# Kernel tuning notes

Hardware: AMD Instinct MI355X
Metric: run time of the kernel (lower is better)

Reference implementation:

```python
import jax, jax.numpy as jnp
import numpy as np

TEMPERATURE = 0.5
B, D = 4096, 256


def setup_inputs() -> dict:
    key = jax.random.key(0)
    k1, k2 = jax.random.split(key)
    z_i = jax.random.normal(k1, (B, D), dtype=jnp.float32)
    z_j = jax.random.normal(k2, (B, D), dtype=jnp.float32)
    return {"z_i": z_i, "z_j": z_j}


def reference(z_i, z_j):
    batch = z_i.shape[0]
    n = 2 * batch
    z = jnp.concatenate([z_i, z_j], axis=0)                      # [2B, D]
    z = z / jnp.linalg.norm(z, axis=1, keepdims=True)            # L2-normalize rows
    # cosine_similarity of unit vectors == dot product -> single GEMM
    sim = jnp.einsum('id,jd->ij', z, z) / TEMPERATURE            # [2B, 2B]
    mask = jnp.eye(n, dtype=bool)
    sim = jnp.where(mask, -jnp.inf, sim)                         # mask self-similarity
    positives = jnp.concatenate(
        [jnp.diagonal(sim, offset=batch), jnp.diagonal(sim, offset=-batch)], axis=0
    )                                                            # [2B]
    loss = -positives + jax.nn.logsumexp(sim, axis=1)            # [2B]
    return loss.mean()
```

## Files before the change

kernel.cpp:

```cpp
#include <hip/hip_runtime.h>
#include <hip/hip_bf16.h>
#include <stdint.h>
#include <stddef.h>


#define B_ROWS 4096
#define D_DIM  256
#define N_ROWS 8192
#define BM 128
#define BN 128

typedef __bf16 bf16;
typedef bf16  bf16x8  __attribute__((ext_vector_type(8)));
typedef bf16  bf16x4  __attribute__((ext_vector_type(4)));
typedef float floatx4 __attribute__((ext_vector_type(4)));

__global__ __launch_bounds__(256) void normalize_kernel(
    const float* __restrict__ z_i, const float* __restrict__ z_j,
    bf16* __restrict__ zn, float* __restrict__ sumexp) {
  const int wave = threadIdx.x >> 6;
  const int lane = threadIdx.x & 63;
  const int row  = blockIdx.x * 4 + wave;
  const float* src = (row < B_ROWS) ? (z_i + (size_t)row * D_DIM)
                                    : (z_j + (size_t)(row - B_ROWS) * D_DIM);
  float4 v = ((const float4*)src)[lane];
  float ss = v.x * v.x + v.y * v.y + v.z * v.z + v.w * v.w;
  #pragma unroll
  for (int m = 1; m < 64; m <<= 1) ss += __shfl_xor(ss, m);
  const float rn = rsqrtf(ss) * 1.6986436f;
  bf16x4 o;
  o[0] = (bf16)(v.x * rn);
  o[1] = (bf16)(v.y * rn);
  o[2] = (bf16)(v.z * rn);
  o[3] = (bf16)(v.w * rn);
  ((bf16x4*)(zn + (size_t)row * D_DIM))[lane] = o;
  if (lane == 0) sumexp[row] = 0.f;
}

__global__ __launch_bounds__(512, 2) void simexp_kernel(
    const bf16* __restrict__ zn, float* __restrict__ sumexp,
    float* __restrict__ pos) {
  __shared__ __align__(16) bf16 Bs[2][BN * D_DIM];

  const int tid   = threadIdx.x;
  const int wave  = tid >> 6;
  const int lane  = tid & 63;
  const int lcol  = lane & 15;
  const int lquad = lane >> 4;
  const int wr = (wave >> 2) * 64;
  const int wc = (wave & 3) * 32;
  const int ri = blockIdx.x >> 2;
  const int cj = blockIdx.x & 3;
  const int row_base = ri * BM;
  const bool has_tail = (ri < 32 && cj >= 2);

  auto ct_of = [&](int t) { return (ri + 8 * cj + t) & 63; };

  auto stageB = [&](int buf, const bf16* src, int it0, int it1) {
    for (int it = it0; it < it1; ++it) {
      const int s   = it * 512 + tid;
      const int n   = s >> 5;
      const int kcs = s & 31;
      const int kc  = (kcs & 24) | ((kcs & 7) ^ (n & 7));
      __builtin_amdgcn_global_load_lds(
          (const __attribute__((address_space(1))) unsigned int*)
              (src + (size_t)n * D_DIM + kc * 8),
          (__attribute__((address_space(3))) unsigned int*)&Bs[buf][s * 8],
          16, 0, 0);
    }
  };

  stageB(0, zn + (size_t)row_base * D_DIM, 0, 8);
  stageB(1, zn + (size_t)ct_of(0) * BM * D_DIM, 0, 8);
  __syncthreads();

  floatx4 af[4][8];
  #pragma unroll
  for (int ti = 0; ti < 4; ++ti) {
    const int n = wr + ti * 16 + lcol;
    #pragma unroll
    for (int kq = 0; kq < 8; ++kq) {
      const int kc  = kq * 4 + lquad;
      const int kcs = (kc & 24) | ((kc & 7) ^ (n & 7));
      af[ti][kq] = *(const floatx4*)(&Bs[0][(n * 32 + kcs) * 8]);
    }
  }
  __syncthreads();

  float rowsum[4][4];
  #pragma unroll
  for (int ti = 0; ti < 4; ++ti)
    #pragma unroll
    for (int r = 0; r < 4; ++r) rowsum[ti][r] = 0.f;

#define MFMA_(A, B_, C) __builtin_amdgcn_mfma_f32_16x16x32_bf16( \
    __builtin_bit_cast(bf16x8, A), B_, C, 0, 0, 0)
#define PHASE(KQA, KQB, IT0, IT1, DO_VM)                                  \
  {                                                                       \
    bf16x8 bfrA[2], bfrB[2];                                              \
    const int kcA = (KQA) * 4 + lquad, kcB = (KQB) * 4 + lquad;           \
    _Pragma("unroll")                                                     \
    for (int tj = 0; tj < 2; ++tj) {                                      \
      const int n  = wc + tj * 16 + lcol;                                 \
      const int sA = (kcA & 24) | ((kcA & 7) ^ (n & 7));                  \
      const int sB = (kcB & 24) | ((kcB & 7) ^ (n & 7));                  \
      bfrA[tj] = *(const bf16x8*)(bbase + n * D_DIM + sA * 8);            \
      bfrB[tj] = *(const bf16x8*)(bbase + n * D_DIM + sB * 8);            \
    }                                                                     \
    stageB(sb, nsrc, IT0, IT1);                                           \
    __builtin_amdgcn_sched_barrier(0);                                    \
    __builtin_amdgcn_s_barrier();                                         \
    asm volatile("s_waitcnt lgkmcnt(0)" ::: "memory");                    \
    __builtin_amdgcn_sched_barrier(0);                                    \
    __builtin_amdgcn_s_setprio(1);                                        \
    _Pragma("unroll")                                                     \
    for (int ti = 0; ti < 4; ++ti) {                                      \
      acc[ti][0] = MFMA_(af[ti][KQA], bfrA[0], acc[ti][0]);               \
      acc[ti][1] = MFMA_(af[ti][KQA], bfrA[1], acc[ti][1]);               \
    }                                                                     \
    _Pragma("unroll")                                                     \
    for (int ti = 0; ti < 4; ++ti) {                                      \
      acc[ti][0] = MFMA_(af[ti][KQB], bfrB[0], acc[ti][0]);               \
      acc[ti][1] = MFMA_(af[ti][KQB], bfrB[1], acc[ti][1]);               \
    }                                                                     \
    __builtin_amdgcn_s_setprio(0);                                        \
    if (DO_VM) asm volatile("s_waitcnt vmcnt(0)" ::: "memory");           \
    __builtin_amdgcn_sched_barrier(0);                                    \
    __builtin_amdgcn_s_barrier();                                         \
  }

  #pragma unroll 1
  for (int t = 0; t < 8; ++t) {
    const int cb = (t ^ 1) & 1;
    const int sb = cb ^ 1;
    const bf16* bbase = &Bs[cb][0];
    const bf16* nsrc = nullptr;
    int nl = 0;
    if (t < 7) {
      nsrc = zn + (size_t)ct_of(t + 1) * BM * D_DIM;
      nl = 8;
    } else if (has_tail) {
      nsrc = zn + (size_t)((ri + 32) * BM + (cj - 2) * 64) * D_DIM;
      nl = 4;
    }
    const int nh = nl >> 1;

    floatx4 acc[4][2];
    #pragma unroll
    for (int ti = 0; ti < 4; ++ti)
      #pragma unroll
      for (int tj = 0; tj < 2; ++tj) acc[ti][tj] = floatx4{0.f, 0.f, 0.f, 0.f};

    PHASE(0, 1, 0, nh, false)
    PHASE(2, 3, nh, nl, false)
    PHASE(4, 5, 0, 0, false)
    PHASE(6, 7, 0, 0, true)

    const bool diag = (cj == 0 && t == 0);
    const int col_base = ct_of(t) * BM;
    float colsum[2] = {0.f, 0.f};
    #pragma unroll
    for (int ti = 0; ti < 4; ++ti) {
      #pragma unroll
      for (int tj = 0; tj < 2; ++tj) {
        #pragma unroll
        for (int r = 0; r < 4; ++r) {
          const float v = acc[ti][tj][r];
          float e = __builtin_amdgcn_exp2f(v);
          if (diag) {
            const int rg = row_base + wr + ti * 16 + lquad * 4 + r;
            const int cg = col_base + wc + tj * 16 + lcol;
            if (cg == rg) e = 0.f;
          }
          rowsum[ti][r] += e;
          colsum[tj]    += e;
        }
      }
    }
    if (!diag) {
      #pragma unroll
      for (int tj = 0; tj < 2; ++tj) {
        float cs = colsum[tj];
        cs += __shfl_xor(cs, 16);
        cs += __shfl_xor(cs, 32);
        if (lquad == 0)
          atomicAdd(&sumexp[col_base + wc + tj * 16 + lcol], cs);
      }
    }
  }

  if (has_tail && wc < 64) {
    const int h = cj - 2;
    const int col_base = (ri + 32) * BM + h * 64;
    const bf16* bbase = &Bs[1][0];
    floatx4 acc[4][2];
    #pragma unroll
    for (int ti = 0; ti < 4; ++ti)
      #pragma unroll
      for (int tj = 0; tj < 2; ++tj) acc[ti][tj] = floatx4{0.f, 0.f, 0.f, 0.f};
    #pragma unroll
    for (int kq = 0; kq < 8; ++kq) {
      const int kc = kq * 4 + lquad;
      bf16x8 bfr[2];
      #pragma unroll
      for (int tj = 0; tj < 2; ++tj) {
        const int n   = wc + tj * 16 + lcol;
        const int kcs = (kc & 24) | ((kc & 7) ^ (n & 7));
        bfr[tj] = *(const bf16x8*)(bbase + n * D_DIM + kcs * 8);
      }
      #pragma unroll
      for (int ti = 0; ti < 4; ++ti) {
        acc[ti][0] = MFMA_(af[ti][kq], bfr[0], acc[ti][0]);
        acc[ti][1] = MFMA_(af[ti][kq], bfr[1], acc[ti][1]);
      }
    }
    float colsum[2] = {0.f, 0.f};
    #pragma unroll
    for (int ti = 0; ti < 4; ++ti) {
      #pragma unroll
      for (int tj = 0; tj < 2; ++tj) {
        #pragma unroll
        for (int r = 0; r < 4; ++r) {
          const float v = acc[ti][tj][r];
          const float e = __builtin_amdgcn_exp2f(v);
          const int rg = row_base + wr + ti * 16 + lquad * 4 + r;
          const int cg = col_base + wc + tj * 16 + lcol;
          if (cg == rg + B_ROWS) {
            const float p = v * 0.6931471805599453f;
            pos[rg] = p;
            pos[cg] = p;
          }
          rowsum[ti][r] += e;
          colsum[tj]    += e;
        }
      }
    }
    #pragma unroll
    for (int tj = 0; tj < 2; ++tj) {
      float cs = colsum[tj];
      cs += __shfl_xor(cs, 16);
      cs += __shfl_xor(cs, 32);
      if (lquad == 0)
        atomicAdd(&sumexp[col_base + wc + tj * 16 + lcol], cs);
    }
  }
#undef PHASE
#undef MFMA_

  #pragma unroll
  for (int ti = 0; ti < 4; ++ti) {
    #pragma unroll
    for (int r = 0; r < 4; ++r) {
      float s2 = rowsum[ti][r];
      s2 += __shfl_xor(s2, 1);
      s2 += __shfl_xor(s2, 2);
      s2 += __shfl_xor(s2, 4);
      s2 += __shfl_xor(s2, 8);
      if (lcol == 0) {
        const int grow = row_base + wr + ti * 16 + lquad * 4 + r;
        atomicAdd(&sumexp[grow], s2);
      }
    }
  }
}

__global__ __launch_bounds__(1024) void reduce_kernel(
    const float* __restrict__ sumexp, const float* __restrict__ pos,
    float* __restrict__ out) {
  __shared__ float ws[16];
  const int tid = threadIdx.x;
  float s = 0.f;
  const float ln2 = 0.6931471805599453f;
  for (int k = tid; k < N_ROWS; k += 1024)
    s += __builtin_amdgcn_logf(sumexp[k]) * ln2 - pos[k];
  #pragma unroll
  for (int m = 1; m < 64; m <<= 1) s += __shfl_xor(s, m);
  const int wave = tid >> 6, lane = tid & 63;
  if (lane == 0) ws[wave] = s;
  __syncthreads();
  if (wave == 0) {
    float t = (lane < 16) ? ws[lane] : 0.f;
    #pragma unroll
    for (int m = 1; m < 16; m <<= 1) t += __shfl_xor(t, m);
    if (lane == 0) out[0] = t * (1.0f / N_ROWS);
  }
}

extern "C" void kernel_launch(void* const* d_in, const int* in_sizes, int n_in,
                              void* d_out, int out_size, void* d_ws,
                              size_t ws_size, hipStream_t stream) {
  const float* z_i = (const float*)d_in[0];
  const float* z_j = (const float*)d_in[1];
  float* out = (float*)d_out;

  bf16* zn = (bf16*)d_ws;
  float* sumexp = (float*)((char*)d_ws + (size_t)N_ROWS * D_DIM * sizeof(bf16));
  float* pos = sumexp + N_ROWS;

  normalize_kernel<<<N_ROWS / 4, 256, 0, stream>>>(z_i, z_j, zn, sumexp);
  simexp_kernel<<<256, 512, 0, stream>>>(zn, sumexp, pos);
  reduce_kernel<<<1, 1024, 0, stream>>>(sumexp, pos, out);
}
```

Measured before the change: 92.55 us.

## Overlap previous tile's exp epilogue with next tile's MFMA phases

Double-buffers the accumulator tile (accA/accB) and unrolls the column-tile loop by two. The exp2, row-sum and column-sum epilogue of the previous tile is split into per-ti slices interleaved into the four MFMA phases of the current tile, with a drain after the loop. The aim is to hide transcendental and ALU epilogue work behind matrix-core execution. The cost is roughly double the accumulator registers, which may raise VGPR pressure and lower occupancy.

```diff
diff --git a/kernel.cpp b/kernel.cpp
--- a/kernel.cpp
+++ b/kernel.cpp
@@ -93,9 +93,34 @@
     #pragma unroll
     for (int r = 0; r < 4; ++r) rowsum[ti][r] = 0.f;
 
+  floatx4 accA[4][2], accB[4][2];
+  float pcs0 = 0.f, pcs1 = 0.f;
+  int   pcol  = 0;
+  bool  pdiag = false;
+
 #define MFMA_(A, B_, C) __builtin_amdgcn_mfma_f32_16x16x32_bf16( \
     __builtin_bit_cast(bf16x8, A), B_, C, 0, 0, 0)
-#define PHASE(KQA, KQB, IT0, IT1, DO_VM)                                  \
+
+#define SLICE(ACCP, TI, PV)                                               \
+    if (PV) {                                                             \
+      _Pragma("unroll")                                                   \
+      for (int tj = 0; tj < 2; ++tj) {                                    \
+        _Pragma("unroll")                                                 \
+        for (int r = 0; r < 4; ++r) {                                     \
+          const float v = ACCP[TI][tj][r];                                \
+          float e = __builtin_amdgcn_exp2f(v);                            \
+          if (pdiag) {                                                    \
+            const int rg = row_base + wr + (TI) * 16 + lquad * 4 + r;     \
+            const int cg = pcol + wc + tj * 16 + lcol;                    \
+            if (cg == rg) e = 0.f;              \
+          }                                                               \
+          rowsum[TI][r] += e;                                             \
+          if (tj == 0) pcs0 += e; else pcs1 += e;                         \
+        }                                                                 \
+      }                                                                   \
+    }
+
+#define PHASE(ACCC, ACCP, PV, KQA, KQB, IT0, IT1, DO_VM, TI)              \
   {                                                                       \
     bf16x8 bfrA[2], bfrB[2];                                              \
     const int kcA = (KQA) * 4 + lquad, kcB = (KQB) * 4 + lquad;           \
@@ -115,83 +140,86 @@
     __builtin_amdgcn_s_setprio(1);                                        \
     _Pragma("unroll")                                                     \
     for (int ti = 0; ti < 4; ++ti) {                                      \
-      acc[ti][0] = MFMA_(af[ti][KQA], bfrA[0], acc[ti][0]);               \
-      acc[ti][1] = MFMA_(af[ti][KQA], bfrA[1], acc[ti][1]);               \
+      ACCC[ti][0] = MFMA_(af[ti][KQA], bfrA[0], ACCC[ti][0]);             \
+      ACCC[ti][1] = MFMA_(af[ti][KQA], bfrA[1], ACCC[ti][1]);             \
     }                                                                     \
     _Pragma("unroll")                                                     \
     for (int ti = 0; ti < 4; ++ti) {                                      \
-      acc[ti][0] = MFMA_(af[ti][KQB], bfrB[0], acc[ti][0]);               \
-      acc[ti][1] = MFMA_(af[ti][KQB], bfrB[1], acc[ti][1]);               \
+      ACCC[ti][0] = MFMA_(af[ti][KQB], bfrB[0], ACCC[ti][0]);             \
+      ACCC[ti][1] = MFMA_(af[ti][KQB], bfrB[1], ACCC[ti][1]);             \
     }                                                                     \
     __builtin_amdgcn_s_setprio(0);                                        \
+    SLICE(ACCP, TI, PV)  \
     if (DO_VM) asm volatile("s_waitcnt vmcnt(0)" ::: "memory");           \
     __builtin_amdgcn_sched_barrier(0);                                    \
     __builtin_amdgcn_s_barrier();                                         \
   }
 
+#define TILE_BODY(ACCC, ACCP, PV, CB, TT)                                 \
+  {                                                                       \
+    const int sb = (CB) ^ 1;                                              \
+    const bf16* bbase = &Bs[CB][0];                                       \
+    const bf16* nsrc = nullptr;                                           \
+    int nl = 0;                                                           \
+    if ((TT) < 7) {                                                       \
+      nsrc = zn + (size_t)ct_of((TT) + 1) * BM * D_DIM;                   \
+      nl = 8;                                                             \
+    } else if (has_tail) {                                                \
+      nsrc = zn + (size_t)((ri + 32) * BM + (cj - 2) * 64) * D_DIM;       \
+      nl = 4;                                                             \
+    }                                                                     \
+    const int nh = nl >> 1;                                               \
+    _Pragma("unroll")                                                     \
+    for (int ti = 0; ti < 4; ++ti) {                                      \
+      ACCC[ti][0] = floatx4{0.f, 0.f, 0.f, 0.f};                          \
+      ACCC[ti][1] = floatx4{0.f, 0.f, 0.f, 0.f};                          \
+    }                                                                     \
+    PHASE(ACCC, ACCP, PV, 0, 1, 0, nh, false, 0)                          \
+    PHASE(ACCC, ACCP, PV, 2, 3, nh, nl, false, 1)                         \
+    PHASE(ACCC, ACCP, PV, 4, 5, 0, 0, false, 2)                           \
+    PHASE(ACCC, ACCP, PV, 6, 7, 0, 0, true, 3)                            \
+    if ((PV) && !pdiag) {          \
+      float c0 = pcs0, c1 = pcs1;                                         \
+      c0 += __shfl_xor(c0, 16); c0 += __shfl_xor(c0, 32);                 \
+      c1 += __shfl_xor(c1, 16); c1 += __shfl_xor(c1, 32);                 \
+      if (lquad == 0) {                                                   \
+        atomicAdd(&sumexp[pcol + wc + lcol], c0);                         \
+        atomicAdd(&sumexp[pcol + wc + 16 + lcol], c1);                    \
+      }                                                                   \
+    }                                                                     \
+    pcol = ct_of(TT) * BM;                                                \
+    pdiag = (cj == 0 && (TT) == 0);                                       \
+    pcs0 = 0.f; pcs1 = 0.f;                                               \
+  }
+
   #pragma unroll 1
-  for (int t = 0; t < 8; ++t) {
-    const int cb = (t ^ 1) & 1;
-    const int sb = cb ^ 1;
-    const bf16* bbase = &Bs[cb][0];
-    const bf16* nsrc = nullptr;
-    int nl = 0;
-    if (t < 7) {
-      nsrc = zn + (size_t)ct_of(t + 1) * BM * D_DIM;
-      nl = 8;
-    } else if (has_tail) {
-      nsrc = zn + (size_t)((ri + 32) * BM + (cj - 2) * 64) * D_DIM;
-      nl = 4;
-    }
-    const int nh = nl >> 1;
-
-    floatx4 acc[4][2];
+  for (int t = 0; t < 8; t += 2) {
+    TILE_BODY(accA, accB, (t > 0), 1, t)
+    TILE_BODY(accB, accA, true, 0, t + 1)
+  }
+
+  {
+    float c0 = 0.f, c1 = 0.f;
     #pragma unroll
     for (int ti = 0; ti < 4; ++ti)
       #pragma unroll
-      for (int tj = 0; tj < 2; ++tj) acc[ti][tj] = floatx4{0.f, 0.f, 0.f, 0.f};
-
-    PHASE(0, 1, 0, nh, false)
-    PHASE(2, 3, nh, nl, false)
-    PHASE(4, 5, 0, 0, false)
-    PHASE(6, 7, 0, 0, true)
-
-    const bool diag = (cj == 0 && t == 0);
-    const int col_base = ct_of(t) * BM;
-    float colsum[2] = {0.f, 0.f};
-    #pragma unroll
-    for (int ti = 0; ti < 4; ++ti) {
-      #pragma unroll
-      for (int tj = 0; tj < 2; ++tj) {
+      for (int tj = 0; tj < 2; ++tj)
         #pragma unroll
         for (int r = 0; r < 4; ++r) {
-          const float v = acc[ti][tj][r];
-          float e = __builtin_amdgcn_exp2f(v);
-          if (diag) {
-            const int rg = row_base + wr + ti * 16 + lquad * 4 + r;
-            const int cg = col_base + wc + tj * 16 + lcol;
-            if (cg == rg) e = 0.f;
-          }
+          const float e = __builtin_amdgcn_exp2f(accB[ti][tj][r]);
           rowsum[ti][r] += e;
-          colsum[tj]    += e;
+          if (tj == 0) c0 += e; else c1 += e;
         }
-      }
-    }
-    if (!diag) {
-      #pragma unroll
-      for (int tj = 0; tj < 2; ++tj) {
-        float cs = colsum[tj];
-        cs += __shfl_xor(cs, 16);
-        cs += __shfl_xor(cs, 32);
-        if (lquad == 0)
-          atomicAdd(&sumexp[col_base + wc + tj * 16 + lcol], cs);
-      }
+    c0 += __shfl_xor(c0, 16); c0 += __shfl_xor(c0, 32);
+    c1 += __shfl_xor(c1, 16); c1 += __shfl_xor(c1, 32);
+    if (lquad == 0) {
+      atomicAdd(&sumexp[pcol + wc + lcol], c0);
+      atomicAdd(&sumexp[pcol + wc + 16 + lcol], c1);
     }
   }
 
   if (has_tail && wc < 64) {
-    const int h = cj - 2;
-    const int col_base = (ri + 32) * BM + h * 64;
+    const int col_base = (ri + 32) * BM + (cj - 2) * 64;
     const bf16* bbase = &Bs[1][0];
     floatx4 acc[4][2];
     #pragma unroll
@@ -214,7 +242,7 @@
         acc[ti][1] = MFMA_(af[ti][kq], bfr[1], acc[ti][1]);
       }
     }
-    float colsum[2] = {0.f, 0.f};
+    float c0 = 0.f, c1 = 0.f;
     #pragma unroll
     for (int ti = 0; ti < 4; ++ti) {
       #pragma unroll
@@ -231,20 +259,20 @@
             pos[cg] = p;
           }
           rowsum[ti][r] += e;
-          colsum[tj]    += e;
+          if (tj == 0) c0 += e; else c1 += e;
         }
       }
     }
-    #pragma unroll
-    for (int tj = 0; tj < 2; ++tj) {
-      float cs = colsum[tj];
-      cs += __shfl_xor(cs, 16);
-      cs += __shfl_xor(cs, 32);
-      if (lquad == 0)
-        atomicAdd(&sumexp[col_base + wc + tj * 16 + lcol], cs);
-    }
-  }
+    c0 += __shfl_xor(c0, 16); c0 += __shfl_xor(c0, 32);
+    c1 += __shfl_xor(c1, 16); c1 += __shfl_xor(c1, 32);
+    if (lquad == 0) {
+      atomicAdd(&sumexp[col_base + wc + lcol], c0);
+      atomicAdd(&sumexp[col_base + wc + 16 + lcol], c1);
+    }
+  }
+#undef TILE_BODY
 #undef PHASE
+#undef SLICE
 #undef MFMA_
 
   #pragma unroll
```

New measurement: 120.7 us. 1.3x slower.
